# Optimization experiments

Measured on AMD Instinct MI355X. Metric: run time of the kernel, lower is better.

## Reference

```python
import jax, jax.numpy as jnp
import numpy as np

# Static config matching init_kwargs
LA = 20.0
GAMMA_INV = 1.0 / 0.1   # self.gamma = 1/gamma
TAU = 0.2
MARGIN = 0.01 * 1.0      # margin * margin_scale
CN = 2
K = 2048
DIM = 128
SUMK = CN * K
B = 16384

# Static intra-class upper-triangular pair mask (same as self.weight in torch)
_blk = np.triu(np.ones((K, K), dtype=bool), k=1)
PAIR_MASK = np.zeros((SUMK, SUMK), dtype=bool)
for _i in range(CN):
    PAIR_MASK[_i * K:(_i + 1) * K, _i * K:(_i + 1) * K] = _blk
PAIR_MASK = jnp.asarray(PAIR_MASK)
N_PAIRS = float(CN * K * (K - 1) // 2)


def setup_inputs() -> dict:
    key = jax.random.key(0)
    k1, k2, k3 = jax.random.split(key, 3)
    x = jax.random.normal(k1, (B, DIM), dtype=jnp.float32)
    target = jax.random.randint(k2, (B,), 0, CN, dtype=jnp.int64)
    fc = jax.random.normal(k3, (DIM, SUMK), dtype=jnp.float32) * 0.05
    return {"x": x, "target": target, "fc": fc}


def reference(x, target, fc):
    # L2-normalize inputs (dim=1) and centers (dim=0)
    norm_input = x / jnp.linalg.norm(x, axis=1, keepdims=True)          # [B, DIM]
    centers = fc / jnp.linalg.norm(fc, axis=0, keepdims=True)           # [DIM, SUMK]

    simInd = norm_input @ centers                                       # [B, SUMK]
    sim = simInd.reshape(B, CN, K)                                      # per-class groups

    # softmax-weighted intra-class similarity (intra_max='softmax')
    prob = jax.nn.softmax(sim * GAMMA_INV, axis=-1)
    simClass = jnp.sum(prob * sim, axis=-1)                             # [B, CN]

    # NOTE: original code sets margin on ALL columns, so uniform shift
    logits = LA * (simClass - MARGIN)

    # cross-entropy, mean reduction (class weights are all 1)
    logp = jax.nn.log_softmax(logits, axis=-1)
    ce = -jnp.take_along_axis(logp, target[:, None].astype(jnp.int32), axis=1).mean()

    # center-pair regularizer (tau > 0, K > 1)
    simCenter = centers.T @ centers                                     # [SUMK, SUMK]
    d = jnp.sqrt(2.0 + 1e-5 - 2.0 * simCenter)                          # >=0 everywhere
    reg = jnp.sum(jnp.where(PAIR_MASK, d, 0.0)) / (N_PAIRS * 2.0)

    loss = ce + TAU * reg
    return loss, logits
```

## Files before the change

kernel.cpp:

```cpp
#include <hip/hip_runtime.h>
#include <math.h>

#define NB 16384
#define DIM 128
#define SUMK 4096
#define KCLS 2048

constexpr float LA = 20.0f;
constexpr float TAU = 0.2f;
constexpr float MARGIN = 0.01f;
constexpr float NPAIRS2 = 8384512.0f;
constexpr float G2L = 14.426950408889634f;
#define CS (8 * NB)

typedef _Float16 half8 __attribute__((ext_vector_type(8)));
typedef float f32x4 __attribute__((ext_vector_type(4)));

#if __has_builtin(__builtin_amdgcn_exp2f)
#define EXP2(v) __builtin_amdgcn_exp2f(v)
#else
#define EXP2(v) exp2f(v)
#endif

#define GLOAD_LDS(SRC, DST)                                                          \
    __builtin_amdgcn_global_load_lds(                                                \
        (const __attribute__((address_space(1))) void*)(SRC),                        \
        (__attribute__((address_space(3))) void*)(DST), 16, 0, 0)

__global__ __launch_bounds__(256) void knorm(const float* __restrict__ fc,
                                             _Float16* __restrict__ cnT) {
    __shared__ float tile[DIM][35];
    const int t = threadIdx.x;
    const int j0 = blockIdx.x * 32;

    const int jr = t & 31;
    const int dr = t >> 5;
#pragma unroll
    for (int it = 0; it < 16; ++it) {
        int d = it * 8 + dr;
        tile[d][jr] = fc[(size_t)d * SUMK + j0 + jr];
    }
    __syncthreads();

    const int p = t & 7;
    const int j = t >> 3;
    float v[16];
    float ss = 0.f;
#pragma unroll
    for (int i = 0; i < 16; ++i) {
        v[i] = tile[p * 16 + i][j];
        ss = fmaf(v[i], v[i], ss);
    }
    ss += __shfl_xor(ss, 1);
    ss += __shfl_xor(ss, 2);
    ss += __shfl_xor(ss, 4);
    float rn = 1.0f / sqrtf(ss);

    _Float16* w = cnT + (size_t)(j0 + j) * DIM + p * 16;
    half8 h0, h1;
#pragma unroll
    for (int k = 0; k < 8; ++k) {
        h0[k] = (_Float16)(v[k] * rn);
        h1[k] = (_Float16)(v[8 + k] * rn);
    }
    *(half8*)w = h0;
    *(half8*)(w + 8) = h1;
}

__global__ __launch_bounds__(256, 4) void kbig(const float* __restrict__ x,
                                               const _Float16* __restrict__ cnT,
                                               float* __restrict__ pw,
                                               float* __restrict__ reg_acc) {
    __shared__ _Float16 smem[3][2][4][64][8];
    __shared__ float red[4];

    const int t = threadIdx.x;
    const int lane = t & 63;
    const int wid = t >> 6;
    const int m = lane & 15;
    const int kg = lane >> 4;
    const int id = blockIdx.x;

    if (id >= 1024) {
        const int rid = id - 1024;
        const int cls = rid >> 10;
        const int ti = (rid >> 5) & 31;
        const int tj = rid & 31;
        if (tj < ti) return;

        const int i0 = cls * KCLS + ti * 64 + wid * 16;
        const int jb = cls * KCLS + tj * 64;

        const _Float16* aip = cnT + (size_t)(i0 + m) * DIM + kg * 8;
        half8 af[4];
#pragma unroll
        for (int tt = 0; tt < 4; ++tt) af[tt] = *(const half8*)(aip + tt * 32);

        half8 bf[16];
#pragma unroll
        for (int fj = 0; fj < 4; ++fj) {
            const _Float16* bjp = cnT + (size_t)(jb + fj * 16 + m) * DIM + kg * 8;
#pragma unroll
            for (int tt = 0; tt < 4; ++tt) bf[fj * 4 + tt] = *(const half8*)(bjp + tt * 32);
        }

        float local = 0.f;
#pragma unroll
        for (int fj = 0; fj < 4; ++fj) {
            f32x4 cc = {0.f, 0.f, 0.f, 0.f};
#pragma unroll
            for (int tt = 0; tt < 4; ++tt)
                cc = __builtin_amdgcn_mfma_f32_16x16x32_f16(af[tt], bf[fj * 4 + tt], cc, 0, 0, 0);
            int gj = jb + fj * 16 + m;
#pragma unroll
            for (int r = 0; r < 4; ++r) {
                int gi = i0 + kg * 4 + r;
                if (gi < gj)
                    local += sqrtf(fmaxf(2.0f + 1e-5f - 2.f * cc[r], 0.f));
            }
        }
#pragma unroll
        for (int off = 1; off < 64; off <<= 1) local += __shfl_xor(local, off);
        if (lane == 0) red[wid] = local;
        __syncthreads();
        if (t == 0) atomicAdd(reg_acc, (red[0] + red[1]) + (red[2] + red[3]));
        return;
    }

    const int cls = (id >> 7) & 1;
    const int qz = id >> 8;
    const int r0 = (id & 127) * 128 + wid * 32;

    half8 b0[4], b1[4];
#define LOADX(ROW, BF)                                                        \
    do {                                                                      \
        const float* xp = x + (size_t)(ROW)*DIM + kg * 8;                     \
        float xr[4][8];                                                       \
        float ss = 0.f;                                                       \
        _Pragma("unroll") for (int tt = 0; tt < 4; ++tt) {                    \
            float4 f0 = *(const float4*)(xp + tt * 32);                       \
            float4 f1 = *(const float4*)(xp + tt * 32 + 4);                   \
            xr[tt][0] = f0.x; xr[tt][1] = f0.y; xr[tt][2] = f0.z;             \
            xr[tt][3] = f0.w; xr[tt][4] = f1.x; xr[tt][5] = f1.y;             \
            xr[tt][6] = f1.z; xr[tt][7] = f1.w;                               \
            _Pragma("unroll") for (int qq = 0; qq < 8; ++qq)                  \
                ss = fmaf(xr[tt][qq], xr[tt][qq], ss);                        \
        }                                                                     \
        ss += __shfl_xor(ss, 16);                                             \
        ss += __shfl_xor(ss, 32);                                             \
        float rn = G2L / sqrtf(ss);                                           \
        _Pragma("unroll") for (int tt = 0; tt < 4; ++tt)                      \
            _Pragma("unroll") for (int qq = 0; qq < 8; ++qq)                  \
                BF[tt][qq] = (_Float16)(xr[tt][qq] * rn);                     \
    } while (0)

    LOADX(r0 + m, b0);
    LOADX(r0 + 16 + m, b1);
#undef LOADX

    const int q0 = wid * 2, q1 = wid * 2 + 1;
    const int cf0 = q0 >> 2, tt0 = q0 & 3;
    const int cf1 = q1 >> 2, tt1 = q1 & 3;
    const int colbase = cls * KCLS + qz * 512;
    const _Float16* s0 = cnT + (size_t)(colbase + cf0 * 16 + m) * DIM + tt0 * 32 + kg * 8;
    const _Float16* s1 = cnT + (size_t)(colbase + cf1 * 16 + m) * DIM + tt1 * 32 + kg * 8;
    const size_t CSTEP = (size_t)32 * DIM;

#define STAGE(CH, BUF)                                                    \
    do {                                                                  \
        GLOAD_LDS(s0 + (size_t)(CH) * CSTEP, &smem[BUF][cf0][tt0][0][0]); \
        GLOAD_LDS(s1 + (size_t)(CH) * CSTEP, &smem[BUF][cf1][tt1][0][0]); \
    } while (0)

    float rz0 = 0.f, rw0 = 0.f, rz1 = 0.f, rw1 = 0.f;

#define EPI(C, RZ, RW)                                                        \
    do {                                                                      \
        float e0 = EXP2(C[0]);                                                \
        float e1 = EXP2(C[1]);                                                \
        float e2 = EXP2(C[2]);                                                \
        float e3 = EXP2(C[3]);                                                \
        RZ += (e0 + e1) + (e2 + e3);                                          \
        RW += fmaf(e0, C[0], e1 * C[1]) + fmaf(e2, C[2], e3 * C[3]);          \
    } while (0)

#define COMPUTE(B)                                                            \
    do {                                                                      \
        _Pragma("unroll") for (int cf = 0; cf < 2; ++cf) {                    \
            half8 a0 = *(const half8*)&smem[B][cf][0][lane][0];               \
            half8 a1 = *(const half8*)&smem[B][cf][1][lane][0];               \
            half8 a2 = *(const half8*)&smem[B][cf][2][lane][0];               \
            half8 a3 = *(const half8*)&smem[B][cf][3][lane][0];               \
            f32x4 c0 = {0.f, 0.f, 0.f, 0.f}, c1 = {0.f, 0.f, 0.f, 0.f};      \
            c0 = __builtin_amdgcn_mfma_f32_16x16x32_f16(a0, b0[0], c0, 0, 0, 0); \
            c1 = __builtin_amdgcn_mfma_f32_16x16x32_f16(a0, b1[0], c1, 0, 0, 0); \
            c0 = __builtin_amdgcn_mfma_f32_16x16x32_f16(a1, b0[1], c0, 0, 0, 0); \
            c1 = __builtin_amdgcn_mfma_f32_16x16x32_f16(a1, b1[1], c1, 0, 0, 0); \
            c0 = __builtin_amdgcn_mfma_f32_16x16x32_f16(a2, b0[2], c0, 0, 0, 0); \
            c1 = __builtin_amdgcn_mfma_f32_16x16x32_f16(a2, b1[2], c1, 0, 0, 0); \
            c0 = __builtin_amdgcn_mfma_f32_16x16x32_f16(a3, b0[3], c0, 0, 0, 0); \
            c1 = __builtin_amdgcn_mfma_f32_16x16x32_f16(a3, b1[3], c1, 0, 0, 0); \
            EPI(c0, rz0, rw0);                                                \
            EPI(c1, rz1, rw1);                                                \
        }                                                                     \
    } while (0)

    STAGE(0, 0);
    STAGE(1, 1);

    for (int ch = 0; ch < 15; ++ch) {
        asm volatile("s_waitcnt vmcnt(2)" ::: "memory");
        __builtin_amdgcn_s_barrier();
        if (ch < 14) STAGE(ch + 2, (ch + 2) % 3);
        COMPUTE(ch % 3);
    }
    asm volatile("s_waitcnt vmcnt(0)" ::: "memory");
    __builtin_amdgcn_s_barrier();
    COMPUTE(0);
#undef COMPUTE
#undef EPI
#undef STAGE

    rz0 += __shfl_xor(rz0, 16); rz0 += __shfl_xor(rz0, 32);
    rw0 += __shfl_xor(rw0, 16); rw0 += __shfl_xor(rw0, 32);
    rz1 += __shfl_xor(rz1, 16); rz1 += __shfl_xor(rz1, 32);
    rw1 += __shfl_xor(rw1, 16); rw1 += __shfl_xor(rw1, 32);

    if (lane < 16) {
        const size_t base = (size_t)(cls * 4 + qz) * NB;
        const int rowA = r0 + m, rowB = r0 + 16 + m;
        pw[0 * CS + base + rowA] = rz0;
        pw[0 * CS + base + rowB] = rz1;
        pw[1 * CS + base + rowA] = rw0;
        pw[1 * CS + base + rowB] = rw1;
    }
}

__global__ __launch_bounds__(256) void kce(const float* __restrict__ pw,
                                           const int* __restrict__ tgt,
                                           float* __restrict__ out,
                                           float* __restrict__ accum) {
    __shared__ float red2[4];
    const int t = threadIdx.x;
    int i = blockIdx.x * 256 + t;
    float lg[2];
#pragma unroll
    for (int cls = 0; cls < 2; ++cls) {
        float z = 0.f, w = 0.f;
#pragma unroll
        for (int q = 0; q < 4; ++q) {
            const size_t base = (size_t)(cls * 4 + q) * NB + i;
            z += pw[0 * CS + base];
            w += pw[1 * CS + base];
        }
        lg[cls] = LA * (w / (z * G2L) - MARGIN);
        out[1 + 2 * i + cls] = lg[cls];
    }
    int tg = tgt[i];
    float mx = fmaxf(lg[0], lg[1]);
    float lse = mx + logf(expf(lg[0] - mx) + expf(lg[1] - mx));
    float ce = lse - (tg ? lg[1] : lg[0]);
#pragma unroll
    for (int off = 1; off < 64; off <<= 1) ce += __shfl_xor(ce, off);
    if ((t & 63) == 0) red2[t >> 6] = ce;
    __syncthreads();
    if (t == 0) {
        atomicAdd(&accum[0], (red2[0] + red2[1]) + (red2[2] + red2[3]));
        __threadfence();
        unsigned old = atomicAdd((unsigned*)&accum[2], 1u);
        if (old == (unsigned)(NB / 256 - 1)) {
            float ce_tot = atomicAdd(&accum[0], 0.0f);
            float reg    = atomicAdd(&accum[1], 0.0f);
            out[0] = ce_tot / (float)NB + TAU * (reg / NPAIRS2);
        }
    }
}

extern "C" void kernel_launch(void* const* d_in, const int* in_sizes, int n_in,
                              void* d_out, int out_size, void* d_ws, size_t ws_size,
                              hipStream_t stream) {
    const float* x  = (const float*)d_in[0];
    const int*   tg = (const int*)d_in[1];
    const float* fc = (const float*)d_in[2];
    float* out = (float*)d_out;
    float* ws  = (float*)d_ws;
    float* accum = ws;
    _Float16* cnT = (_Float16*)(ws + 16);
    float* pw = (float*)(cnT + (size_t)SUMK * DIM);

    hipMemsetAsync(accum, 0, 64, stream);
    knorm<<<SUMK / 32, 256, 0, stream>>>(fc, cnT);
    kbig<<<1024 + 2048, 256, 0, stream>>>(x, cnT, pw, accum + 1);
    kce<<<NB / 256, 256, 0, stream>>>(pw, tg, out, accum);
}
```

Baseline: 112.9 us.

## Fuse CE epilogue into main kernel and retile to 64 rows per wave

Each wave now handles 64 x rows against 256 columns instead of 32 rows against 512, so every LDS-staged center tile is reused across four row fragments. Block indices are reordered so the 16 blocks sharing a 256-row band finish together. The separate cross-entropy kernel is removed: the last block per row band, found through a per-band atomic counter, reduces the partials and computes logits and CE, and a global counter finalizes the loss. This trades more registers and a larger partial buffer plus extra atomics for one fewer launch and fewer LDS reads per MFMA.

```diff
diff --git a/kernel.cpp b/kernel.cpp
--- a/kernel.cpp
+++ b/kernel.cpp
@@ -11,7 +11,7 @@
 constexpr float MARGIN = 0.01f;
 constexpr float NPAIRS2 = 8384512.0f;
 constexpr float G2L = 14.426950408889634f;
-#define CS (8 * NB)
+#define CS (16 * NB)
 
 typedef _Float16 half8 __attribute__((ext_vector_type(8)));
 typedef float f32x4 __attribute__((ext_vector_type(4)));
@@ -69,10 +69,18 @@
 
 __global__ __launch_bounds__(256, 4) void kbig(const float* __restrict__ x,
                                                const _Float16* __restrict__ cnT,
+                                               const int* __restrict__ tgt,
                                                float* __restrict__ pw,
-                                               float* __restrict__ reg_acc) {
+                                               float* __restrict__ out,
+                                               float* __restrict__ wsf) {
     __shared__ _Float16 smem[3][2][4][64][8];
     __shared__ float red[4];
+    __shared__ unsigned sflag;
+
+    float* acc_ce = wsf;
+    float* acc_rg = wsf + 1;
+    unsigned* done = (unsigned*)(wsf + 2);
+    unsigned* rgc  = (unsigned*)(wsf + 3);
 
     const int t = threadIdx.x;
     const int lane = t & 63;
@@ -81,12 +89,27 @@
     const int kg = lane >> 4;
     const int id = blockIdx.x;
 
+#define FINISH_IF_LAST()                                                      \
+    do {                                                                      \
+        __threadfence();                                                      \
+        unsigned old_ = atomicAdd(done, 1u);                                  \
+        if (old_ == 3071u) {                                                  \
+            __threadfence();                                                  \
+            float ce_ = atomicAdd(acc_ce, 0.f);                               \
+            float rg_ = atomicAdd(acc_rg, 0.f);                               \
+            out[0] = ce_ / (float)NB + TAU * (rg_ / NPAIRS2);                 \
+        }                                                                     \
+    } while (0)
+
     if (id >= 1024) {
         const int rid = id - 1024;
         const int cls = rid >> 10;
         const int ti = (rid >> 5) & 31;
         const int tj = rid & 31;
-        if (tj < ti) return;
+        if (tj < ti) {
+            if (t == 0) FINISH_IF_LAST();
+            return;
+        }
 
         const int i0 = cls * KCLS + ti * 64 + wid * 16;
         const int jb = cls * KCLS + tj * 64;
@@ -123,16 +146,20 @@
         for (int off = 1; off < 64; off <<= 1) local += __shfl_xor(local, off);
         if (lane == 0) red[wid] = local;
         __syncthreads();
-        if (t == 0) atomicAdd(reg_acc, (red[0] + red[1]) + (red[2] + red[3]));
+        if (t == 0) {
+            atomicAdd(acc_rg, (red[0] + red[1]) + (red[2] + red[3]));
+            FINISH_IF_LAST();
+        }
         return;
     }
 
-    const int cls = (id >> 7) & 1;
-    const int qz = id >> 8;
-    const int r0 = (id & 127) * 128 + wid * 32;
-
-    half8 b0[4], b1[4];
-#define LOADX(ROW, BF)                                                        \
+    const int rb = id >> 4;
+    const int cls = (id >> 3) & 1;
+    const int qz = id & 7;
+    const int r0 = rb * 256 + wid * 64;
+
+    half8 b[4][4];
+#define LOADX(ROW, RF)                                                        \
     do {                                                                      \
         const float* xp = x + (size_t)(ROW)*DIM + kg * 8;                     \
         float xr[4][8];                                                       \
@@ -151,17 +178,20 @@
         float rn = G2L / sqrtf(ss);                                           \
         _Pragma("unroll") for (int tt = 0; tt < 4; ++tt)                      \
             _Pragma("unroll") for (int qq = 0; qq < 8; ++qq)                  \
-                BF[tt][qq] = (_Float16)(xr[tt][qq] * rn);                     \
-    } while (0)
-
-    LOADX(r0 + m, b0);
-    LOADX(r0 + 16 + m, b1);
+                b[RF][tt][qq] = (_Float16)(xr[tt][qq] * rn);                  \
+    } while (0)
+
+    LOADX(r0 + m, 0);
+    LOADX(r0 + 16 + m, 1);
+    __builtin_amdgcn_sched_barrier(0);
+    LOADX(r0 + 32 + m, 2);
+    LOADX(r0 + 48 + m, 3);
 #undef LOADX
 
     const int q0 = wid * 2, q1 = wid * 2 + 1;
     const int cf0 = q0 >> 2, tt0 = q0 & 3;
     const int cf1 = q1 >> 2, tt1 = q1 & 3;
-    const int colbase = cls * KCLS + qz * 512;
+    const int colbase = cls * KCLS + qz * 256;
     const _Float16* s0 = cnT + (size_t)(colbase + cf0 * 16 + m) * DIM + tt0 * 32 + kg * 8;
     const _Float16* s1 = cnT + (size_t)(colbase + cf1 * 16 + m) * DIM + tt1 * 32 + kg * 8;
     const size_t CSTEP = (size_t)32 * DIM;
@@ -172,7 +202,8 @@
         GLOAD_LDS(s1 + (size_t)(CH) * CSTEP, &smem[BUF][cf1][tt1][0][0]); \
     } while (0)
 
-    float rz0 = 0.f, rw0 = 0.f, rz1 = 0.f, rw1 = 0.f;
+    float rz[4] = {0.f, 0.f, 0.f, 0.f};
+    float rw[4] = {0.f, 0.f, 0.f, 0.f};
 
 #define EPI(C, RZ, RW)                                                        \
     do {                                                                      \
@@ -191,89 +222,88 @@
             half8 a1 = *(const half8*)&smem[B][cf][1][lane][0];               \
             half8 a2 = *(const half8*)&smem[B][cf][2][lane][0];               \
             half8 a3 = *(const half8*)&smem[B][cf][3][lane][0];               \
-            f32x4 c0 = {0.f, 0.f, 0.f, 0.f}, c1 = {0.f, 0.f, 0.f, 0.f};      \
-            c0 = __builtin_amdgcn_mfma_f32_16x16x32_f16(a0, b0[0], c0, 0, 0, 0); \
-            c1 = __builtin_amdgcn_mfma_f32_16x16x32_f16(a0, b1[0], c1, 0, 0, 0); \
-            c0 = __builtin_amdgcn_mfma_f32_16x16x32_f16(a1, b0[1], c0, 0, 0, 0); \
-            c1 = __builtin_amdgcn_mfma_f32_16x16x32_f16(a1, b1[1], c1, 0, 0, 0); \
-            c0 = __builtin_amdgcn_mfma_f32_16x16x32_f16(a2, b0[2], c0, 0, 0, 0); \
-            c1 = __builtin_amdgcn_mfma_f32_16x16x32_f16(a2, b1[2], c1, 0, 0, 0); \
-            c0 = __builtin_amdgcn_mfma_f32_16x16x32_f16(a3, b0[3], c0, 0, 0, 0); \
-            c1 = __builtin_amdgcn_mfma_f32_16x16x32_f16(a3, b1[3], c1, 0, 0, 0); \
-            EPI(c0, rz0, rw0);                                                \
-            EPI(c1, rz1, rw1);                                                \
+            f32x4 c[4];                                                       \
+            __builtin_amdgcn_s_setprio(1);                                    \
+            _Pragma("unroll") for (int rf = 0; rf < 4; ++rf) {                \
+                f32x4 cc = {0.f, 0.f, 0.f, 0.f};                              \
+                cc = __builtin_amdgcn_mfma_f32_16x16x32_f16(a0, b[rf][0], cc, 0, 0, 0); \
+                cc = __builtin_amdgcn_mfma_f32_16x16x32_f16(a1, b[rf][1], cc, 0, 0, 0); \
+                cc = __builtin_amdgcn_mfma_f32_16x16x32_f16(a2, b[rf][2], cc, 0, 0, 0); \
+                cc = __builtin_amdgcn_mfma_f32_16x16x32_f16(a3, b[rf][3], cc, 0, 0, 0); \
+                c[rf] = cc;                                                   \
+            }                                                                 \
+            __builtin_amdgcn_s_setprio(0);                                    \
+            _Pragma("unroll") for (int rf = 0; rf < 4; ++rf)                  \
+                EPI(c[rf], rz[rf], rw[rf]);                                   \
         }                                                                     \
     } while (0)
 
     STAGE(0, 0);
     STAGE(1, 1);
 
-    for (int ch = 0; ch < 15; ++ch) {
+    for (int ch = 0; ch < 7; ++ch) {
         asm volatile("s_waitcnt vmcnt(2)" ::: "memory");
         __builtin_amdgcn_s_barrier();
-        if (ch < 14) STAGE(ch + 2, (ch + 2) % 3);
+        if (ch < 6) STAGE(ch + 2, (ch + 2) % 3);
         COMPUTE(ch % 3);
     }
     asm volatile("s_waitcnt vmcnt(0)" ::: "memory");
     __builtin_amdgcn_s_barrier();
-    COMPUTE(0);
+    COMPUTE(1);
 #undef COMPUTE
 #undef EPI
 #undef STAGE
 
-    rz0 += __shfl_xor(rz0, 16); rz0 += __shfl_xor(rz0, 32);
-    rw0 += __shfl_xor(rw0, 16); rw0 += __shfl_xor(rw0, 32);
-    rz1 += __shfl_xor(rz1, 16); rz1 += __shfl_xor(rz1, 32);
-    rw1 += __shfl_xor(rw1, 16); rw1 += __shfl_xor(rw1, 32);
+#pragma unroll
+    for (int rf = 0; rf < 4; ++rf) {
+        rz[rf] += __shfl_xor(rz[rf], 16); rz[rf] += __shfl_xor(rz[rf], 32);
+        rw[rf] += __shfl_xor(rw[rf], 16); rw[rf] += __shfl_xor(rw[rf], 32);
+    }
 
     if (lane < 16) {
-        const size_t base = (size_t)(cls * 4 + qz) * NB;
-        const int rowA = r0 + m, rowB = r0 + 16 + m;
-        pw[0 * CS + base + rowA] = rz0;
-        pw[0 * CS + base + rowB] = rz1;
-        pw[1 * CS + base + rowA] = rw0;
-        pw[1 * CS + base + rowB] = rw1;
-    }
-}
-
-__global__ __launch_bounds__(256) void kce(const float* __restrict__ pw,
-                                           const int* __restrict__ tgt,
-                                           float* __restrict__ out,
-                                           float* __restrict__ accum) {
-    __shared__ float red2[4];
-    const int t = threadIdx.x;
-    int i = blockIdx.x * 256 + t;
-    float lg[2];
-#pragma unroll
-    for (int cls = 0; cls < 2; ++cls) {
-        float z = 0.f, w = 0.f;
-#pragma unroll
-        for (int q = 0; q < 4; ++q) {
-            const size_t base = (size_t)(cls * 4 + q) * NB + i;
-            z += pw[0 * CS + base];
-            w += pw[1 * CS + base];
-        }
-        lg[cls] = LA * (w / (z * G2L) - MARGIN);
-        out[1 + 2 * i + cls] = lg[cls];
-    }
-    int tg = tgt[i];
-    float mx = fmaxf(lg[0], lg[1]);
-    float lse = mx + logf(expf(lg[0] - mx) + expf(lg[1] - mx));
-    float ce = lse - (tg ? lg[1] : lg[0]);
-#pragma unroll
-    for (int off = 1; off < 64; off <<= 1) ce += __shfl_xor(ce, off);
-    if ((t & 63) == 0) red2[t >> 6] = ce;
+        const size_t base = (size_t)(cls * 8 + qz) * NB;
+#pragma unroll
+        for (int rf = 0; rf < 4; ++rf) {
+            const int row = r0 + rf * 16 + m;
+            pw[0 * CS + base + row] = rz[rf];
+            pw[1 * CS + base + row] = rw[rf];
+        }
+    }
+
+    __threadfence();
+    if (t == 0) {
+        unsigned old = atomicAdd(&rgc[rb], 1u);
+        unsigned last = (old == 15u) ? 1u : 0u;
+        if (last) __threadfence();
+        sflag = last;
+    }
     __syncthreads();
-    if (t == 0) {
-        atomicAdd(&accum[0], (red2[0] + red2[1]) + (red2[2] + red2[3]));
-        __threadfence();
-        unsigned old = atomicAdd((unsigned*)&accum[2], 1u);
-        if (old == (unsigned)(NB / 256 - 1)) {
-            float ce_tot = atomicAdd(&accum[0], 0.0f);
-            float reg    = atomicAdd(&accum[1], 0.0f);
-            out[0] = ce_tot / (float)NB + TAU * (reg / NPAIRS2);
-        }
-    }
+    if (sflag) {
+        const int i = rb * 256 + t;
+        float z0 = 0.f, w0 = 0.f, z1 = 0.f, w1 = 0.f;
+#pragma unroll
+        for (int q = 0; q < 8; ++q) {
+            z0 += pw[0 * CS + (size_t)q * NB + i];
+            w0 += pw[1 * CS + (size_t)q * NB + i];
+            z1 += pw[0 * CS + (size_t)(8 + q) * NB + i];
+            w1 += pw[1 * CS + (size_t)(8 + q) * NB + i];
+        }
+        float lg0 = LA * (w0 / (z0 * G2L) - MARGIN);
+        float lg1 = LA * (w1 / (z1 * G2L) - MARGIN);
+        out[1 + 2 * i] = lg0;
+        out[2 + 2 * i] = lg1;
+        int tg = tgt[i];
+        float mx = fmaxf(lg0, lg1);
+        float lse = mx + logf(expf(lg0 - mx) + expf(lg1 - mx));
+        float ce = lse - (tg ? lg1 : lg0);
+#pragma unroll
+        for (int off = 1; off < 64; off <<= 1) ce += __shfl_xor(ce, off);
+        if ((t & 63) == 0) red[t >> 6] = ce;
+        __syncthreads();
+        if (t == 0) atomicAdd(acc_ce, (red[0] + red[1]) + (red[2] + red[3]));
+    }
+    if (t == 0) FINISH_IF_LAST();
+#undef FINISH_IF_LAST
 }
 
 extern "C" void kernel_launch(void* const* d_in, const int* in_sizes, int n_in,
@@ -284,12 +314,10 @@
     const float* fc = (const float*)d_in[2];
     float* out = (float*)d_out;
     float* ws  = (float*)d_ws;
-    float* accum = ws;
-    _Float16* cnT = (_Float16*)(ws + 16);
+    _Float16* cnT = (_Float16*)(ws + 256);
     float* pw = (float*)(cnT + (size_t)SUMK * DIM);
 
-    hipMemsetAsync(accum, 0, 64, stream);
+    hipMemsetAsync(ws, 0, 1024, stream);
     knorm<<<SUMK / 32, 256, 0, stream>>>(fc, cnT);
-    kbig<<<1024 + 2048, 256, 0, stream>>>(x, cnT, pw, accum + 1);
-    kce<<<NB / 256, 256, 0, stream>>>(pw, tg, out, accum);
+    kbig<<<1024 + 2048, 256, 0, stream>>>(x, cnT, tg, pw, out, ws);
 }
```

Result: slower. 245.5 us (+117.4%).
